# Performance work log

Measured on AMD Instinct MI355X. Metric: run time of the kernel, lower is better.

The kernel has to match this reference:

```python
import jax, jax.numpy as jnp
import numpy as np

ALPHA = 0.15       # blend weight for merged mean vs center token
SIZE_DELTA = 0.0   # additive smoothing on cluster sizes


def setup_inputs() -> dict:
    key = jax.random.key(0)
    B, T, C = 8, 4096, 1024
    x = jax.random.normal(key, (B, T, C), dtype=jnp.float32)
    return {"x": x, "layer_idx": 0, "requested_r": 2048}


def reference(x, layer_idx, requested_r):
    B, T, C = x.shape
    K = max(1, T - int(requested_r))

    # token importance scores = squared L2 norm per token
    scores = jnp.sum(x * x, axis=-1)                      # [B, T]
    # CLS protection: force token 0 to be kept
    scores = scores.at[:, 0].set(jnp.finfo(scores.dtype).max)
    _, keep_idx = jax.lax.top_k(scores, K)                # [B, K]
    keep_idx = jnp.sort(keep_idx, axis=-1)

    # cosine nearest-kept-center assignment
    feat = x / (jnp.linalg.norm(x, axis=-1, keepdims=True) + 1e-12)  # [B, T, C]
    kept_feat = jnp.take_along_axis(feat, keep_idx[..., None], axis=1)  # [B, K, C]
    sim = jnp.einsum('bth,bkh->btk', feat, kept_feat)     # [B, T, K]
    assign_idx = jnp.argmax(sim, axis=-1)                 # [B, T]
    # force each kept center to self-assign (vectorized scatter,
    # replaces the original Python double for-loop with .item() syncs)
    b_idx = jnp.arange(B)[:, None]
    assign_idx = assign_idx.at[b_idx, keep_idx].set(jnp.arange(K)[None, :])

    # scatter-based size-weighted merge: segment mean over assigned tokens
    seg = (assign_idx + jnp.arange(B)[:, None] * K).reshape(-1)       # [B*T]
    sums = jax.ops.segment_sum(x.reshape(B * T, C), seg, num_segments=B * K)
    cnt = jax.ops.segment_sum(jnp.ones((B * T,), x.dtype), seg, num_segments=B * K)
    merged = (sums / (cnt[:, None] + SIZE_DELTA)).reshape(B, K, C)    # [B, K, C]

    x_kept = jnp.take_along_axis(x, keep_idx[..., None], axis=1)      # [B, K, C]
    out = (1.0 - ALPHA) * x_kept + ALPHA * merged
    return out
```

## Files before the change

### kernel.cpp

```cpp
#include <hip/hip_runtime.h>
#include <hip/hip_bf16.h>
#include <float.h>
#include <math.h>

constexpr int B_ = 8;
constexpr int T_ = 4096;
constexpr int C_ = 1024;
constexpr int K_ = 2048;
constexpr int MROWS = T_ - K_;

constexpr int BM = 128, BN = 128, BK = 32;
constexpr int NB = K_ / BN;
constexpr float REFINE_DELTA = 4e-4f;

typedef _Float16 f16x8 __attribute__((ext_vector_type(8)));
typedef float    f32x4 __attribute__((ext_vector_type(4)));

__device__ __forceinline__ void gload16(const ushort* g, ushort* l) {
  __builtin_amdgcn_global_load_lds(
      (const __attribute__((address_space(1))) unsigned int*)g,
      (__attribute__((address_space(3))) unsigned int*)l, 16, 0, 0);
}

__global__ __launch_bounds__(256) void split_score_kernel(
    const float* __restrict__ x, ushort* __restrict__ xh,
    double* __restrict__ sd, float* __restrict__ rnorm)
{
  int row = blockIdx.x;
  size_t base = (size_t)row * C_;
  int i4 = threadIdx.x * 4;
  float4 v = *reinterpret_cast<const float4*>(&x[base + i4]);
  ushort4 h;
  { _Float16 a = (_Float16)v.x; h.x = *(ushort*)&a; }
  { _Float16 a = (_Float16)v.y; h.y = *(ushort*)&a; }
  { _Float16 a = (_Float16)v.z; h.z = *(ushort*)&a; }
  { _Float16 a = (_Float16)v.w; h.w = *(ushort*)&a; }
  *reinterpret_cast<ushort4*>(&xh[base + i4]) = h;
  double s = (double)v.x * v.x + (double)v.y * v.y
           + (double)v.z * v.z + (double)v.w * v.w;
  #pragma unroll
  for (int off = 32; off > 0; off >>= 1) s += __shfl_down(s, off);
  __shared__ double ws4[4];
  int lane = threadIdx.x & 63, wave = threadIdx.x >> 6;
  if (lane == 0) ws4[wave] = s;
  __syncthreads();
  if (threadIdx.x == 0) {
    double t = ws4[0] + ws4[1] + ws4[2] + ws4[3];
    sd[row] = t;
    rnorm[row] = (float)(1.0 / (sqrt(t) + 1e-12));
  }
}

__global__ __launch_bounds__(256) void rank_kernel(
    const double* __restrict__ sd, int* __restrict__ flag)
{
  int b = blockIdx.y;
  __shared__ double sh[T_];
  for (int i = threadIdx.x; i < T_; i += 256)
    sh[i] = (i == 0) ? DBL_MAX : sd[b * T_ + i];
  __syncthreads();
  int t = blockIdx.x * 128 + (threadIdx.x >> 1);
  int half = threadIdx.x & 1;
  double key = sh[t];
  int cnt = 0;
  int j0 = half * 2048;
  #pragma unroll 4
  for (int jj = 0; jj < 2048; jj++) {
    int j = j0 + jj;
    double sj = sh[j];
    cnt += (sj > key) || (sj == key && j < t);
  }
  cnt += __shfl_xor(cnt, 1);
  if (half == 0) flag[b * T_ + t] = (cnt < K_) ? 1 : 0;
}

__global__ __launch_bounds__(256) void select_kernel(
    const int* __restrict__ flag, int* __restrict__ keep_idx,
    int* __restrict__ drop_idx, int* __restrict__ assign)
{
  int b = blockIdx.x, tid = threadIdx.x;
  __shared__ int sums[256];
  int f[16], s = 0;
  int base = b * T_ + tid * 16;
  #pragma unroll
  for (int i = 0; i < 16; i++) { f[i] = flag[base + i]; s += f[i]; }
  sums[tid] = s;
  __syncthreads();
  for (int off = 1; off < 256; off <<= 1) {
    int v = 0;
    if (tid >= off) v = sums[tid - off];
    __syncthreads();
    if (tid >= off) sums[tid] += v;
    __syncthreads();
  }
  int run = (tid == 0) ? 0 : sums[tid - 1];
  #pragma unroll
  for (int i = 0; i < 16; i++) {
    int t = tid * 16 + i;
    if (f[i]) { keep_idx[b * K_ + run] = t; assign[b * T_ + t] = run; run++; }
    else drop_idx[b * MROWS + (t - run)] = t;
  }
}

__global__ void zero_kernel(int* __restrict__ cnt, int* __restrict__ nref)
{
  int i = blockIdx.x * 256 + threadIdx.x;
  if (i < B_ * K_) cnt[i] = 0;
  if (i == 0) *nref = 0;
}

__global__ __launch_bounds__(256) void mfma_argmax_kernel(
    const ushort* __restrict__ xh, const float* __restrict__ rnorm,
    const int* __restrict__ keep_idx, const int* __restrict__ drop_idx,
    float* __restrict__ pb, float* __restrict__ ps, int* __restrict__ pk)
{
  __shared__ __align__(16) ushort lds[2][2][4][128][8];

  int b  = blockIdx.z;
  int m0 = blockIdx.y * BM;
  int n0 = blockIdx.x * BN;
  int tid = threadIdx.x;
  int lane = tid & 63, wave = tid >> 6;
  int quad = lane >> 4, col = lane & 15;
  int wm = wave >> 1, wn = wave & 1;

  int srow = tid & 127;
  int sc8  = (tid >> 7) * 8;

  int dtok_s = drop_idx[b * MROWS + m0 + srow];
  const ushort* ga = xh + (size_t)(b * T_ + dtok_s) * C_;
  int ktok_s = keep_idx[b * K_ + n0 + srow];
  const ushort* gb = xh + (size_t)(b * T_ + ktok_s) * C_;

  int ldst = tid * 8;

  float scale[4]; int ncand[4];
  #pragma unroll
  for (int j = 0; j < 4; j++) {
    int nn = n0 + wn * 64 + j * 16 + col;
    ncand[j] = nn;
    scale[j] = rnorm[b * T_ + keep_idx[b * K_ + nn]];
  }

  f32x4 acc[4][4];
  #pragma unroll
  for (int i = 0; i < 4; i++)
    #pragma unroll
    for (int j = 0; j < 4; j++) acc[i][j] = (f32x4)0.f;

  auto issue = [&](int k0, int st) {
    ushort* base = &lds[st][0][0][0][0];
    gload16(ga + k0 + sc8,      base + ldst);
    gload16(ga + k0 + 16 + sc8, base + ldst + 2048);
    gload16(gb + k0 + sc8,      base + 4096 + ldst);
    gload16(gb + k0 + 16 + sc8, base + 4096 + ldst + 2048);
  };

  issue(0, 0);
  __syncthreads();

  for (int ks = 0; ks < C_ / BK; ks++) {
    int cur = ks & 1;
    if (ks < C_ / BK - 1) issue((ks + 1) * BK, cur ^ 1);

    f16x8 fa[4], fb[4];
    #pragma unroll
    for (int i = 0; i < 4; i++) {
      int row = wm * 64 + i * 16 + col;
      fa[i] = *reinterpret_cast<const f16x8*>(&lds[cur][0][quad][row][0]);
    }
    #pragma unroll
    for (int j = 0; j < 4; j++) {
      int row = wn * 64 + j * 16 + col;
      fb[j] = *reinterpret_cast<const f16x8*>(&lds[cur][1][quad][row][0]);
    }
    #pragma unroll
    for (int i = 0; i < 4; i++)
      #pragma unroll
      for (int j = 0; j < 4; j++)
        acc[i][j] = __builtin_amdgcn_mfma_f32_16x16x32_f16(fa[i], fb[j], acc[i][j], 0, 0, 0);
    __syncthreads();
  }

  float* redb   = (float*)(&lds[0][0][0][0][0]);
  float* redsec = redb + 256;
  int*   redk   = (int*)(redb + 512);

  #pragma unroll
  for (int i = 0; i < 4; i++) {
    #pragma unroll
    for (int r = 0; r < 4; r++) {
      float b1 = -FLT_MAX, b2 = -FLT_MAX; int k1 = 0;
      #pragma unroll
      for (int j = 0; j < 4; j++) {
        float v = acc[i][j][r] * scale[j];
        if (v > b1) { b2 = b1; b1 = v; k1 = ncand[j]; }
        else if (v > b2) b2 = v;
      }
      #pragma unroll
      for (int off = 1; off < 16; off <<= 1) {
        float ob1 = __shfl_xor(b1, off);
        float ob2 = __shfl_xor(b2, off);
        int   ok1 = __shfl_xor(k1, off);
        if (ob1 > b1 || (ob1 == b1 && ok1 < k1)) { b2 = fmaxf(b1, ob2); b1 = ob1; k1 = ok1; }
        else b2 = fmaxf(b2, ob1);
      }
      if (col == 0) {
        int tl = wm * 64 + i * 16 + quad * 4 + r;
        redb[wn * 128 + tl] = b1; redsec[wn * 128 + tl] = b2; redk[wn * 128 + tl] = k1;
      }
    }
  }
  __syncthreads();
  if (tid < 128) {
    float b1 = redb[tid], b2 = redsec[tid]; int k1 = redk[tid];
    float o1 = redb[128 + tid], o2 = redsec[128 + tid]; int ok = redk[128 + tid];
    if (o1 > b1) { b2 = fmaxf(b1, o2); b1 = o1; k1 = ok; }
    else b2 = fmaxf(b2, o1);
    size_t p = ((size_t)(b * NB + blockIdx.x)) * MROWS + m0 + tid;
    pb[p] = b1; ps[p] = b2; pk[p] = k1;
  }
}

__global__ __launch_bounds__(256) void reduce2_kernel(
    const float* __restrict__ pb, const float* __restrict__ ps, const int* __restrict__ pk,
    const float* __restrict__ rnorm, const int* __restrict__ drop_idx,
    int* __restrict__ assign, int* __restrict__ rlist, int* __restrict__ nref)
{
  int idx2 = blockIdx.x * 256 + threadIdx.x;
  int b = idx2 >> 11;
  int rc = idx2 & (MROWS - 1);
  float b1 = -FLT_MAX, b2 = -FLT_MAX; int k1 = 0;
  for (int nb = 0; nb < NB; nb++) {
    size_t p = ((size_t)(b * NB + nb)) * MROWS + rc;
    float v = pb[p], s = ps[p]; int k = pk[p];
    if (v > b1) { b2 = fmaxf(b1, s); b1 = v; k1 = k; }
    else b2 = fmaxf(b2, v);
  }
  int t = drop_idx[idx2];
  assign[b * T_ + t] = k1;
  if ((b1 - b2) * rnorm[b * T_ + t] < REFINE_DELTA) {
    int qi = atomicAdd(nref, 1);
    rlist[qi] = idx2;
  }
}

__global__ __launch_bounds__(256) void refine_kernel(
    const float* __restrict__ x, const double* __restrict__ sd,
    const int* __restrict__ keep_idx, const int* __restrict__ drop_idx,
    const float* __restrict__ rnorm,
    const float* __restrict__ pb, const float* __restrict__ ps, const int* __restrict__ pk,
    const int* __restrict__ nref, const int* __restrict__ rlist, int* __restrict__ assign)
{
  __shared__ __align__(16) float xs[C_];
  __shared__ int cand[K_];
  __shared__ int ncand_s;
  __shared__ double wv[4];
  __shared__ int wk[4];
  int n = *nref;
  int lane = threadIdx.x & 63, wave = threadIdx.x >> 6;
  for (int qi = blockIdx.x; qi < n; qi += gridDim.x) {
    int idx2 = rlist[qi];
    int b = idx2 >> 11, rc = idx2 & (MROWS - 1);
    int t = drop_idx[idx2];
    int bt = b * T_ + t;
    __syncthreads();
    const float* xt = x + ((size_t)b * T_ + t) * C_;
    for (int i = threadIdx.x; i < C_; i += 256) xs[i] = xt[i];
    if (threadIdx.x == 0) {
      float b1 = -FLT_MAX;
      for (int nb = 0; nb < NB; nb++) {
        float v = pb[((size_t)(b * NB + nb)) * MROWS + rc];
        if (v > b1) b1 = v;
      }
      float thr = b1 - REFINE_DELTA / rnorm[bt];
      int nc = 0;
      for (int nb = 0; nb < NB; nb++) {
        size_t p = ((size_t)(b * NB + nb)) * MROWS + rc;
        if (pb[p] >= thr) {
          if (ps[p] >= thr) { for (int j = 0; j < BN; j++) cand[nc++] = nb * BN + j; }
          else cand[nc++] = pk[p];
        }
      }
      ncand_s = nc;
    }
    __syncthreads();
    int nc = ncand_s;
    double bv = -DBL_MAX; int bk = 0x7fffffff;
    for (int ci = wave; ci < nc; ci += 4) {
      int k = cand[ci];
      int kt = keep_idx[b * K_ + k];
      const float* xr = x + ((size_t)b * T_ + kt) * C_;
      double s = 0.0;
      int c0 = lane * 16;
      #pragma unroll
      for (int c = 0; c < 16; c += 4) {
        float4 v = *reinterpret_cast<const float4*>(&xr[c0 + c]);
        s += (double)xs[c0 + c]     * v.x + (double)xs[c0 + c + 1] * v.y
           + (double)xs[c0 + c + 2] * v.z + (double)xs[c0 + c + 3] * v.w;
      }
      #pragma unroll
      for (int off = 32; off > 0; off >>= 1) s += __shfl_down(s, off);
      s = __shfl(s, 0);
      s /= sqrt(sd[b * T_ + kt]);
      if (s > bv || (s == bv && k < bk)) { bv = s; bk = k; }
    }
    if (lane == 0) { wv[wave] = bv; wk[wave] = bk; }
    __syncthreads();
    if (threadIdx.x == 0) {
      double fb = wv[0]; int fk = wk[0];
      for (int w2 = 1; w2 < 4; w2++)
        if (wv[w2] > fb || (wv[w2] == fb && wk[w2] < fk)) { fb = wv[w2]; fk = wk[w2]; }
      assign[bt] = fk;
    }
  }
}

__global__ void count_kernel(const int* __restrict__ assign, int* __restrict__ cnt)
{
  int i = blockIdx.x * 256 + threadIdx.x;
  int b = i >> 12;
  atomicAdd(&cnt[b * K_ + assign[i]], 1);
}

__global__ __launch_bounds__(256) void scan_kernel(
    const int* __restrict__ cnt, int* __restrict__ offs, int* __restrict__ cursor)
{
  int b = blockIdx.x, tid = threadIdx.x;
  __shared__ int sums[256];
  int v[8], s = 0;
  int base = b * K_ + tid * 8;
  #pragma unroll
  for (int i = 0; i < 8; i++) { v[i] = cnt[base + i]; s += v[i]; }
  sums[tid] = s;
  __syncthreads();
  for (int off = 1; off < 256; off <<= 1) {
    int t2 = 0;
    if (tid >= off) t2 = sums[tid - off];
    __syncthreads();
    if (tid >= off) sums[tid] += t2;
    __syncthreads();
  }
  int run = (tid == 0) ? 0 : sums[tid - 1];
  #pragma unroll
  for (int i = 0; i < 8; i++) { offs[base + i] = run; cursor[base + i] = run; run += v[i]; }
}

__global__ void scatter_kernel(const int* __restrict__ assign,
                               int* __restrict__ cursor, int* __restrict__ lists)
{
  int i = blockIdx.x * 256 + threadIdx.x;
  int b = i >> 12, t = i & (T_ - 1);
  int p = atomicAdd(&cursor[b * K_ + assign[i]], 1);
  lists[b * T_ + p] = t;
}

__global__ __launch_bounds__(256) void merge_kernel(
    const float* __restrict__ x, const int* __restrict__ keep_idx,
    const int* __restrict__ cnt, const int* __restrict__ offs,
    const int* __restrict__ lists, float* __restrict__ out)
{
  int b = blockIdx.y, k = blockIdx.x;
  int m = cnt[b * K_ + k], off = offs[b * K_ + k];
  const float* xb = x + (size_t)b * T_ * C_;
  int c4 = threadIdx.x * 4;
  float sx = 0.f, sy = 0.f, sz = 0.f, sw = 0.f;
  for (int i = 0; i < m; i++) {
    int tok = lists[b * T_ + off + i];
    float4 v = *reinterpret_cast<const float4*>(&xb[(size_t)tok * C_ + c4]);
    sx += v.x; sy += v.y; sz += v.z; sw += v.w;
  }
  int kt = keep_idx[b * K_ + k];
  float4 xk = *reinterpret_cast<const float4*>(&xb[(size_t)kt * C_ + c4]);
  float fm = (float)m;
  float4 o;
  o.x = 0.85f * xk.x + 0.15f * (sx / fm);
  o.y = 0.85f * xk.y + 0.15f * (sy / fm);
  o.z = 0.85f * xk.z + 0.15f * (sz / fm);
  o.w = 0.85f * xk.w + 0.15f * (sw / fm);
  *reinterpret_cast<float4*>(&out[((size_t)b * K_ + k) * C_ + c4]) = o;
}

extern "C" void kernel_launch(void* const* d_in, const int* in_sizes, int n_in,
                              void* d_out, int out_size, void* d_ws, size_t ws_size,
                              hipStream_t stream)
{
  const float* x = (const float*)d_in[0];
  float* out = (float*)d_out;

  char* w = (char*)d_ws;
  ushort* xh    = (ushort*)w;  w += sizeof(ushort) * (size_t)B_ * T_ * C_;
  float* pb     = (float*)w;   w += sizeof(float) * (size_t)B_ * NB * MROWS;
  float* ps     = (float*)w;   w += sizeof(float) * (size_t)B_ * NB * MROWS;
  int*   pk     = (int*)w;     w += sizeof(int) * (size_t)B_ * NB * MROWS;
  double* sd    = (double*)w;  w += sizeof(double) * B_ * T_;
  float* rnorm  = (float*)w;   w += sizeof(float) * B_ * T_;
  int* flag     = (int*)w;     w += sizeof(int) * B_ * T_;
  int* keep_idx = (int*)w;     w += sizeof(int) * B_ * K_;
  int* drop_idx = (int*)w;     w += sizeof(int) * B_ * MROWS;
  int* assign   = (int*)w;     w += sizeof(int) * B_ * T_;
  int* cnt      = (int*)w;     w += sizeof(int) * B_ * K_;
  int* offs     = (int*)w;     w += sizeof(int) * B_ * K_;
  int* cursor   = (int*)w;     w += sizeof(int) * B_ * K_;
  int* lists    = (int*)w;     w += sizeof(int) * B_ * T_;
  int* rlist    = (int*)w;     w += sizeof(int) * B_ * MROWS;
  int* nref     = (int*)w;     w += 256;

  split_score_kernel<<<B_ * T_, 256, 0, stream>>>(x, xh, sd, rnorm);
  rank_kernel<<<dim3(T_ / 128, B_), 256, 0, stream>>>(sd, flag);
  select_kernel<<<B_, 256, 0, stream>>>(flag, keep_idx, drop_idx, assign);
  zero_kernel<<<(B_ * K_ + 255) / 256, 256, 0, stream>>>(cnt, nref);
  mfma_argmax_kernel<<<dim3(NB, MROWS / BM, B_), 256, 0, stream>>>(
      xh, rnorm, keep_idx, drop_idx, pb, ps, pk);
  reduce2_kernel<<<B_ * MROWS / 256, 256, 0, stream>>>(
      pb, ps, pk, rnorm, drop_idx, assign, rlist, nref);
  refine_kernel<<<256, 256, 0, stream>>>(
      x, sd, keep_idx, drop_idx, rnorm, pb, ps, pk, nref, rlist, assign);
  count_kernel<<<B_ * T_ / 256, 256, 0, stream>>>(assign, cnt);
  scan_kernel<<<B_, 256, 0, stream>>>(cnt, offs, cursor);
  scatter_kernel<<<B_ * T_ / 256, 256, 0, stream>>>(assign, cursor, lists);
  merge_kernel<<<dim3(K_, B_), 256, 0, stream>>>(x, keep_idx, cnt, offs, lists, out);
}
```

Before: 558.1 us.

## Double GEMM K-tile, row-per-wave scoring, and LDS staging in refine and merge

The MFMA argmax kernel now uses a K tile of 64 instead of 32, which halves the number of barriers and loop iterations but doubles the LDS footprint. The split/score kernel assigns one wave per row, so the block-level shared-memory reduction and barrier are gone. The refine kernel loads its per-row partial results into shared memory in parallel instead of having one thread read them serially from global memory. The merge kernel stages token indices in LDS in chunks instead of having every thread read them from global memory.

```diff
diff --git a/kernel.cpp b/kernel.cpp
--- a/kernel.cpp
+++ b/kernel.cpp
@@ -9,7 +9,7 @@
 constexpr int K_ = 2048;
 constexpr int MROWS = T_ - K_;
 
-constexpr int BM = 128, BN = 128, BK = 32;
+constexpr int BM = 128, BN = 128, BK = 64;
 constexpr int NB = K_ / BN;
 constexpr float REFINE_DELTA = 4e-4f;
 
@@ -26,28 +26,28 @@
     const float* __restrict__ x, ushort* __restrict__ xh,
     double* __restrict__ sd, float* __restrict__ rnorm)
 {
-  int row = blockIdx.x;
+  int lane = threadIdx.x & 63, wave = threadIdx.x >> 6;
+  int row = blockIdx.x * 4 + wave;
   size_t base = (size_t)row * C_;
-  int i4 = threadIdx.x * 4;
-  float4 v = *reinterpret_cast<const float4*>(&x[base + i4]);
-  ushort4 h;
-  { _Float16 a = (_Float16)v.x; h.x = *(ushort*)&a; }
-  { _Float16 a = (_Float16)v.y; h.y = *(ushort*)&a; }
-  { _Float16 a = (_Float16)v.z; h.z = *(ushort*)&a; }
-  { _Float16 a = (_Float16)v.w; h.w = *(ushort*)&a; }
-  *reinterpret_cast<ushort4*>(&xh[base + i4]) = h;
-  double s = (double)v.x * v.x + (double)v.y * v.y
-           + (double)v.z * v.z + (double)v.w * v.w;
+  double s = 0.0;
+  #pragma unroll
+  for (int j = 0; j < 4; j++) {
+    int i4 = j * 256 + lane * 4;
+    float4 v = *reinterpret_cast<const float4*>(&x[base + i4]);
+    ushort4 h;
+    { _Float16 a = (_Float16)v.x; h.x = *(ushort*)&a; }
+    { _Float16 a = (_Float16)v.y; h.y = *(ushort*)&a; }
+    { _Float16 a = (_Float16)v.z; h.z = *(ushort*)&a; }
+    { _Float16 a = (_Float16)v.w; h.w = *(ushort*)&a; }
+    *reinterpret_cast<ushort4*>(&xh[base + i4]) = h;
+    s += (double)v.x * v.x + (double)v.y * v.y
+       + (double)v.z * v.z + (double)v.w * v.w;
+  }
   #pragma unroll
   for (int off = 32; off > 0; off >>= 1) s += __shfl_down(s, off);
-  __shared__ double ws4[4];
-  int lane = threadIdx.x & 63, wave = threadIdx.x >> 6;
-  if (lane == 0) ws4[wave] = s;
-  __syncthreads();
-  if (threadIdx.x == 0) {
-    double t = ws4[0] + ws4[1] + ws4[2] + ws4[3];
-    sd[row] = t;
-    rnorm[row] = (float)(1.0 / (sqrt(t) + 1e-12));
+  if (lane == 0) {
+    sd[row] = s;
+    rnorm[row] = (float)(1.0 / (sqrt(s) + 1e-12));
   }
 }
 
@@ -114,7 +114,7 @@
     const int* __restrict__ keep_idx, const int* __restrict__ drop_idx,
     float* __restrict__ pb, float* __restrict__ ps, int* __restrict__ pk)
 {
-  __shared__ __align__(16) ushort lds[2][2][4][128][8];
+  __shared__ __align__(16) ushort lds[2][2][8][128][8];
 
   int b  = blockIdx.z;
   int m0 = blockIdx.y * BM;
@@ -152,8 +152,13 @@
     ushort* base = &lds[st][0][0][0][0];
     gload16(ga + k0 + sc8,      base + ldst);
     gload16(ga + k0 + 16 + sc8, base + ldst + 2048);
-    gload16(gb + k0 + sc8,      base + 4096 + ldst);
-    gload16(gb + k0 + 16 + sc8, base + 4096 + ldst + 2048);
+    gload16(ga + k0 + 32 + sc8, base + ldst + 4096);
+    gload16(ga + k0 + 48 + sc8, base + ldst + 6144);
+    ushort* bb = base + 8192;
+    gload16(gb + k0 + sc8,      bb + ldst);
+    gload16(gb + k0 + 16 + sc8, bb + ldst + 2048);
+    gload16(gb + k0 + 32 + sc8, bb + ldst + 4096);
+    gload16(gb + k0 + 48 + sc8, bb + ldst + 6144);
   };
 
   issue(0, 0);
@@ -163,22 +168,25 @@
     int cur = ks & 1;
     if (ks < C_ / BK - 1) issue((ks + 1) * BK, cur ^ 1);
 
-    f16x8 fa[4], fb[4];
     #pragma unroll
-    for (int i = 0; i < 4; i++) {
-      int row = wm * 64 + i * 16 + col;
-      fa[i] = *reinterpret_cast<const f16x8*>(&lds[cur][0][quad][row][0]);
-    }
-    #pragma unroll
-    for (int j = 0; j < 4; j++) {
-      int row = wn * 64 + j * 16 + col;
-      fb[j] = *reinterpret_cast<const f16x8*>(&lds[cur][1][quad][row][0]);
-    }
-    #pragma unroll
-    for (int i = 0; i < 4; i++)
-      #pragma unroll
-      for (int j = 0; j < 4; j++)
-        acc[i][j] = __builtin_amdgcn_mfma_f32_16x16x32_f16(fa[i], fb[j], acc[i][j], 0, 0, 0);
+    for (int s = 0; s < 2; s++) {
+      f16x8 fa[4], fb[4];
+      #pragma unroll
+      for (int i = 0; i < 4; i++) {
+        int row = wm * 64 + i * 16 + col;
+        fa[i] = *reinterpret_cast<const f16x8*>(&lds[cur][0][s * 4 + quad][row][0]);
+      }
+      #pragma unroll
+      for (int j = 0; j < 4; j++) {
+        int row = wn * 64 + j * 16 + col;
+        fb[j] = *reinterpret_cast<const f16x8*>(&lds[cur][1][s * 4 + quad][row][0]);
+      }
+      #pragma unroll
+      for (int i = 0; i < 4; i++)
+        #pragma unroll
+        for (int j = 0; j < 4; j++)
+          acc[i][j] = __builtin_amdgcn_mfma_f32_16x16x32_f16(fa[i], fb[j], acc[i][j], 0, 0, 0);
+    }
     __syncthreads();
   }
 
@@ -257,6 +265,8 @@
   __shared__ int ncand_s;
   __shared__ double wv[4];
   __shared__ int wk[4];
+  __shared__ float spb[NB], sps[NB];
+  __shared__ int spk[NB];
   int n = *nref;
   int lane = threadIdx.x & 63, wave = threadIdx.x >> 6;
   for (int qi = blockIdx.x; qi < n; qi += gridDim.x) {
@@ -267,19 +277,20 @@
     __syncthreads();
     const float* xt = x + ((size_t)b * T_ + t) * C_;
     for (int i = threadIdx.x; i < C_; i += 256) xs[i] = xt[i];
+    if (threadIdx.x < NB) {
+      size_t p = ((size_t)(b * NB + threadIdx.x)) * MROWS + rc;
+      spb[threadIdx.x] = pb[p]; sps[threadIdx.x] = ps[p]; spk[threadIdx.x] = pk[p];
+    }
+    __syncthreads();
     if (threadIdx.x == 0) {
       float b1 = -FLT_MAX;
-      for (int nb = 0; nb < NB; nb++) {
-        float v = pb[((size_t)(b * NB + nb)) * MROWS + rc];
-        if (v > b1) b1 = v;
-      }
+      for (int nb = 0; nb < NB; nb++) if (spb[nb] > b1) b1 = spb[nb];
       float thr = b1 - REFINE_DELTA / rnorm[bt];
       int nc = 0;
       for (int nb = 0; nb < NB; nb++) {
-        size_t p = ((size_t)(b * NB + nb)) * MROWS + rc;
-        if (pb[p] >= thr) {
-          if (ps[p] >= thr) { for (int j = 0; j < BN; j++) cand[nc++] = nb * BN + j; }
-          else cand[nc++] = pk[p];
+        if (spb[nb] >= thr) {
+          if (sps[nb] >= thr) { for (int j = 0; j < BN; j++) cand[nc++] = nb * BN + j; }
+          else cand[nc++] = spk[nb];
         }
       }
       ncand_s = nc;
@@ -360,15 +371,22 @@
     const int* __restrict__ cnt, const int* __restrict__ offs,
     const int* __restrict__ lists, float* __restrict__ out)
 {
+  __shared__ int toks[256];
   int b = blockIdx.y, k = blockIdx.x;
   int m = cnt[b * K_ + k], off = offs[b * K_ + k];
   const float* xb = x + (size_t)b * T_ * C_;
   int c4 = threadIdx.x * 4;
   float sx = 0.f, sy = 0.f, sz = 0.f, sw = 0.f;
-  for (int i = 0; i < m; i++) {
-    int tok = lists[b * T_ + off + i];
-    float4 v = *reinterpret_cast<const float4*>(&xb[(size_t)tok * C_ + c4]);
-    sx += v.x; sy += v.y; sz += v.z; sw += v.w;
+  for (int basei = 0; basei < m; basei += 256) {
+    int nchunk = min(256, m - basei);
+    __syncthreads();
+    if (threadIdx.x < nchunk) toks[threadIdx.x] = lists[b * T_ + off + basei + threadIdx.x];
+    __syncthreads();
+    for (int i = 0; i < nchunk; i++) {
+      int tok = toks[i];
+      float4 v = *reinterpret_cast<const float4*>(&xb[(size_t)tok * C_ + c4]);
+      sx += v.x; sy += v.y; sz += v.z; sw += v.w;
+    }
   }
   int kt = keep_idx[b * K_ + k];
   float4 xk = *reinterpret_cast<const float4*>(&xb[(size_t)kt * C_ + c4]);
@@ -406,7 +424,7 @@
   int* rlist    = (int*)w;     w += sizeof(int) * B_ * MROWS;
   int* nref     = (int*)w;     w += 256;
 
-  split_score_kernel<<<B_ * T_, 256, 0, stream>>>(x, xh, sd, rnorm);
+  split_score_kernel<<<B_ * T_ / 4, 256, 0, stream>>>(x, xh, sd, rnorm);
   rank_kernel<<<dim3(T_ / 128, B_), 256, 0, stream>>>(sd, flag);
   select_kernel<<<B_, 256, 0, stream>>>(flag, keep_idx, drop_idx, assign);
   zero_kernel<<<(B_ * K_ + 255) / 256, 256, 0, stream>>>(cnt, nref);
```

Result: slower. 574.8 us (+3.0%).
